# Kernel optimization log

Hardware: AMD Instinct MI355X
Metric: run time of the kernel (lower is better)

## Reference

```python
import jax, jax.numpy as jnp
import numpy as np

B, S, D = 8, 4096, 192
MEM_READ, MEM_WRITE, MEM_READY = 156, 157, 158


def setup_inputs() -> dict:
    key = jax.random.key(0)
    ks = jax.random.split(key, 9)
    inp = {"x": jax.random.normal(ks[0], (B, S, D), dtype=jnp.float32)}
    names = ["Wq_r", "Wk_r", "Wv_r", "Wo_r", "Wq_w", "Wk_w", "Wv_w", "Wo_w"]
    for i, n in enumerate(names):
        inp[n] = jax.random.normal(ks[i + 1], (D, D), dtype=jnp.float32) * 0.02
    return inp


def _attention(x, Wq, Wk, Wv, Wo):
    # single-head, non-causal PureAttention: q/k/v = x @ W.T, softmax(qk^T/sqrt(D)) v, then W_o
    q = jnp.einsum('bsd,ed->bse', x, Wq)
    k = jnp.einsum('bsd,ed->bse', x, Wk)
    v = jnp.einsum('bsd,ed->bse', x, Wv)
    scale = jnp.asarray(1.0 / np.sqrt(D), x.dtype)
    scores = jnp.einsum('bqe,bke->bqk', q, k) * scale  # [B,S,S]
    attn = jax.nn.softmax(scores, axis=-1)
    o = jnp.einsum('bqk,bke->bqe', attn, v)
    return jnp.einsum('bse,oe->bso', o, Wo)


def reference(x, Wq_r, Wk_r, Wv_r, Wo_r, Wq_w, Wk_w, Wv_w, Wo_w):
    read_flag = x[:, 0, MEM_READ]    # [B]
    write_flag = x[:, 0, MEM_WRITE]  # [B]
    read_res = _attention(x, Wq_r, Wk_r, Wv_r, Wo_r)
    write_res = _attention(x, Wq_w, Wk_w, Wv_w, Wo_w)
    rg = read_flag[:, None, None]
    wg = write_flag[:, None, None]
    out = x + rg * (read_res - x) + wg * (write_res - x)
    out = out.at[:, :, MEM_READ].set(0.0)
    out = out.at[:, :, MEM_WRITE].set(0.0)
    ready = (read_flag + write_flag)[:, None]  # broadcast over seq
    out = out.at[:, :, MEM_READY].set(jnp.broadcast_to(ready, out.shape[:2]))
    return out
```

## Files before the change

kernel.cpp:

```cpp
#include <hip/hip_runtime.h>
#include <stdint.h>

#define B_ 8
#define S_ 4096
#define D_ 192
#define M_ (B_*S_)

typedef short v8s __attribute__((ext_vector_type(8)));
typedef float v4f __attribute__((ext_vector_type(4)));
typedef unsigned short v4us __attribute__((ext_vector_type(4)));

static __device__ __forceinline__ unsigned short f2bf(float f){
  union{float f; unsigned u;} v; v.f=f;
  unsigned u = v.u;
  unsigned r = (u + 0x7fffu + ((u>>16)&1u))>>16;
  return (unsigned short)r;
}
static __device__ __forceinline__ float fexp2(float x){
  return __builtin_amdgcn_exp2f(x);
}
static __device__ __forceinline__ unsigned cvtpk(float lo, float hi){
  unsigned r;
  asm("v_cvt_pk_bf16_f32 %0, %1, %2" : "=v"(r) : "v"(lo), "v"(hi));
  return r;
}

typedef const __attribute__((address_space(1))) unsigned int gu32;
typedef __attribute__((address_space(3))) unsigned int lu32;
#define GLL16(gp, lp) __builtin_amdgcn_global_load_lds((gu32*)(gp), (lu32*)(lp), 16, 0, 0)

__global__ void cvt_w_kernel(const float* w0,const float* w1,const float* w2,const float* w3,
                             const float* w4,const float* w5,const float* w6,const float* w7,
                             unsigned short* dst){
  int w = blockIdx.y;
  const float* src;
  switch(w){
    case 0: src=w0; break; case 1: src=w1; break; case 2: src=w2; break; case 3: src=w3; break;
    case 4: src=w4; break; case 5: src=w5; break; case 6: src=w6; break; default: src=w7; break;
  }
  int i = blockIdx.x*256 + threadIdx.x;
  float v = src[i];
  if(w==0 || w==4) v *= 0.10411754211316668f;
  dst[(size_t)w*36864 + i] = f2bf(v);
}

__global__ __launch_bounds__(256) void proj_kernel(
    const float* __restrict__ x, const unsigned short* __restrict__ Wb,
    unsigned short* __restrict__ QKV)
{
  __shared__ __align__(16) unsigned short Vstage[192*72];
  const size_t MD = (size_t)M_*D_;
  int tid = threadIdx.x;
  int wid = tid>>6, lane = tid&63;
  int lr = lane&15, lg = lane>>4, kb = lg*8;
  int m0 = blockIdx.x*64 + wid*16;
  int row = m0 + lr;

  v8s a[6];
  #pragma unroll
  for(int c=0;c<6;c++){
    const float* xp = &x[(size_t)row*D_ + c*32 + kb];
    float4 f0 = *(const float4*)xp;
    float4 f1 = *(const float4*)(xp+4);
    v8s t;
    t[0]=(short)f2bf(f0.x); t[1]=(short)f2bf(f0.y); t[2]=(short)f2bf(f0.z); t[3]=(short)f2bf(f0.w);
    t[4]=(short)f2bf(f1.x); t[5]=(short)f2bf(f1.y); t[6]=(short)f2bf(f1.z); t[7]=(short)f2bf(f1.w);
    a[c]=t;
  }
  int bidx = m0 / S_;
  int sb   = (blockIdx.x*64) % S_;
  int sloc = wid*16 + lg*4;

  for(int path=0; path<2; path++){
    unsigned short* dstQ = QKV + (size_t)path*3*MD;
    for(int which=0; which<2; which++){
      const unsigned short* W = Wb + (size_t)(path*4 + which)*36864;
      unsigned short* dst = which==0 ? dstQ : dstQ + MD;
      #pragma unroll
      for(int nt=0; nt<12; nt++){
        v4f acc = {0.f,0.f,0.f,0.f};
        int n = nt*16 + lr;
        #pragma unroll
        for(int c=0;c<6;c++){
          v8s bfr = *(const v8s*)&W[(size_t)n*D_ + c*32 + kb];
          acc = __builtin_amdgcn_mfma_f32_16x16x32_bf16(a[c], bfr, acc, 0,0,0);
        }
        int col = nt*16 + lr;
        int r0 = m0 + lg*4;
        #pragma unroll
        for(int r=0;r<4;r++) dst[(size_t)(r0+r)*D_ + col] = f2bf(acc[r]);
      }
    }
    {
      const unsigned short* W = Wb + (size_t)(path*4 + 2)*36864;
      #pragma unroll
      for(int nt=0; nt<12; nt++){
        v4f acc = {0.f,0.f,0.f,0.f};
        int n = nt*16 + lr;
        #pragma unroll
        for(int c=0;c<6;c++){
          v8s bfr = *(const v8s*)&W[(size_t)n*D_ + c*32 + kb];
          acc = __builtin_amdgcn_mfma_f32_16x16x32_bf16(a[c], bfr, acc, 0,0,0);
        }
        int col = nt*16 + lr;
        v4us pk;
        pk[0]=f2bf(acc[0]); pk[1]=f2bf(acc[1]); pk[2]=f2bf(acc[2]); pk[3]=f2bf(acc[3]);
        *(v4us*)&Vstage[col*72 + sloc] = pk;
      }
      __syncthreads();
      unsigned short* dstV = dstQ + 2*MD;
      size_t vg = (size_t)bidx*D_*S_ + sb;
      #pragma unroll
      for(int j=0;j<6;j++){
        int i = tid + j*256;
        int d = i>>3, s8 = (i&7)*8;
        *(v8s*)&dstV[vg + (size_t)d*S_ + s8] = *(const v8s*)&Vstage[d*72 + s8];
      }
      __syncthreads();
    }
  }
}

__global__ __launch_bounds__(256,2) void attn_kernel(unsigned short* __restrict__ QKV)
{
  __shared__ __align__(16) unsigned short Kb[2][32*192];
  __shared__ __align__(16) unsigned short Vb[3][192*32];

  int flat = blockIdx.x + 32*blockIdx.y + 256*blockIdx.z;
  int w = (flat&7)*64 + (flat>>3);
  int qi = w & 31;
  int b  = (w>>5) & 7;
  int z  = w>>8;

  const size_t MD = (size_t)M_*D_;
  size_t poff = (size_t)z*3*MD;
  const unsigned short* Q  = QKV + poff;
  const unsigned short* K  = QKV + poff + MD;
  const unsigned short* Vt = QKV + poff + 2*MD;
  unsigned short* O = QKV + poff;

  int q0 = qi*128;
  int tid = threadIdx.x, wid=tid>>6, lane=tid&63;
  int lr = lane&15, lg = lane>>4, kb = lg*8;
  size_t bbase = (size_t)b*S_*D_;
  const size_t vbase = (size_t)b*D_*S_;
  int qrow0 = q0 + wid*32;

  int koff[3], voff[3];
  #pragma unroll
  for(int j=0;j<3;j++){
    int pb = (wid*3+j)*1024 + lane*16;
    int krow = pb/384, kin = pb%384;
    koff[j] = krow*192 + ((kin ^ ((krow&7)<<4))>>1);
    int vrow = pb>>6,  vin = pb&63;
    voff[j] = vrow*4096 + ((vin ^ (((vrow>>1)&3)<<4))>>1);
  }
  int xk = (lr&7)<<4;
  int kco[6];
  #pragma unroll
  for(int c=0;c<6;c++) kco[c] = ((c*64 + lg*16) ^ xk) >> 1;
  int vro = ((lg*16) ^ (((lr>>1)&3)<<4)) >> 1;

  v8s qf[2][6];
  #pragma unroll
  for(int h=0;h<2;h++){
    size_t qrow = bbase + (size_t)(qrow0 + h*16 + lr)*D_;
    #pragma unroll
    for(int c=0;c<6;c++) qf[h][c] = *(const v8s*)&Q[qrow + c*32 + kb];
  }
  float lsum[2] = {0.f, 0.f};
  v4f oacc[2][12];
  #pragma unroll
  for(int h=0;h<2;h++)
    #pragma unroll
    for(int e=0;e<12;e++) oacc[h][e] = (v4f){0.f,0.f,0.f,0.f};

  auto do_qk = [&](int kcur, v4f sacc[2][2]){
    __builtin_amdgcn_s_setprio(1);
    #pragma unroll
    for(int ct=0; ct<2; ct++){
      v4f s0v = {0.f,0.f,0.f,0.f}, s1v = {0.f,0.f,0.f,0.f};
      #pragma unroll
      for(int c=0;c<6;c++){
        v8s kf = *(const v8s*)&Kb[kcur][(ct*16+lr)*192 + kco[c]];
        s0v = __builtin_amdgcn_mfma_f32_16x16x32_bf16(kf, qf[0][c], s0v, 0,0,0);
        s1v = __builtin_amdgcn_mfma_f32_16x16x32_bf16(kf, qf[1][c], s1v, 0,0,0);
      }
      sacc[0][ct]=s0v; sacc[1][ct]=s1v;
    }
    __builtin_amdgcn_s_setprio(0);
  };
  auto do_softmax = [&](v4f sacc[2][2], v8s pa[2]){
    #pragma unroll
    for(int h=0;h<2;h++){
      float p00=fexp2(sacc[h][0][0]), p01=fexp2(sacc[h][0][1]);
      float p02=fexp2(sacc[h][0][2]), p03=fexp2(sacc[h][0][3]);
      float p10=fexp2(sacc[h][1][0]), p11=fexp2(sacc[h][1][1]);
      float p12=fexp2(sacc[h][1][2]), p13=fexp2(sacc[h][1][3]);
      lsum[h] += ((p00+p01)+(p02+p03)) + ((p10+p11)+(p12+p13));
      unsigned X0=cvtpk(p00,p01), X1=cvtpk(p02,p03);
      unsigned Y0=cvtpk(p10,p11), Y1=cvtpk(p12,p13);
      asm("v_permlane32_swap_b32 %0, %1" : "+v"(Y0), "+v"(X0));
      asm("v_permlane32_swap_b32 %0, %1" : "+v"(Y1), "+v"(X1));
      asm("v_permlane16_swap_b32 %0, %1" : "+v"(Y0), "+v"(X0));
      asm("v_permlane16_swap_b32 %0, %1" : "+v"(Y1), "+v"(X1));
      union{ v8s s; unsigned w[4]; } u;
      u.w[0] = X0;  u.w[1] = X1;  u.w[2] = Y0;  u.w[3] = Y1;
      pa[h] = u.s;
    }
  };
  auto do_pv = [&](int vcur, v8s pa[2]){
    __builtin_amdgcn_s_setprio(1);
    #pragma unroll
    for(int e=0;e<12;e++){
      v8s vbf = *(const v8s*)&Vb[vcur][(e*16+lr)*32 + vro];
      oacc[0][e] = __builtin_amdgcn_mfma_f32_16x16x32_bf16(pa[0], vbf, oacc[0][e], 0,0,0);
      oacc[1][e] = __builtin_amdgcn_mfma_f32_16x16x32_bf16(pa[1], vbf, oacc[1][e], 0,0,0);
    }
    __builtin_amdgcn_s_setprio(0);
  };

  #pragma unroll
  for(int j=0;j<3;j++){
    GLL16(K  + bbase + koff[j], &Kb[0][(wid*3+j)*512]);
    GLL16(Vt + vbase + voff[j], &Vb[0][(wid*3+j)*512]);
  }
  asm volatile("s_waitcnt vmcnt(0)" ::: "memory");
  __syncthreads();

  v8s pa_prev[2];
  {
    v4f sacc[2][2];
    do_qk(0, sacc);
    const unsigned short* kg = K  + bbase + (size_t)6144;
    const unsigned short* vg = Vt + vbase + (size_t)32;
    #pragma unroll
    for(int j=0;j<3;j++){
      GLL16(kg + koff[j], &Kb[1][(wid*3+j)*512]);
      GLL16(vg + voff[j], &Vb[1][(wid*3+j)*512]);
    }
    __builtin_amdgcn_sched_barrier(0);
    do_softmax(sacc, pa_prev);
  }

  for(int t=1; t<128; t++){
    asm volatile("s_waitcnt vmcnt(0)" ::: "memory");
    __syncthreads();
    int kcur = t&1;
    int vprev = (t-1)%3, vnext = (t+1)%3;

    v4f sacc[2][2];
    do_qk(kcur, sacc);

    if(t<127){
      const unsigned short* kg = K  + bbase + (size_t)(t+1)*6144;
      const unsigned short* vg = Vt + vbase + (size_t)(t+1)*32;
      #pragma unroll
      for(int j=0;j<3;j++){
        GLL16(kg + koff[j], &Kb[(t+1)&1][(wid*3+j)*512]);
        GLL16(vg + voff[j], &Vb[vnext][(wid*3+j)*512]);
      }
    }
    __builtin_amdgcn_sched_barrier(0);

    do_pv(vprev, pa_prev);
    do_softmax(sacc, pa_prev);
  }
  do_pv(127%3, pa_prev);

  float invr[2][4];
  #pragma unroll
  for(int h=0;h<2;h++){
    float ps = lsum[h];
    ps += __shfl_xor(ps, 16);
    ps += __shfl_xor(ps, 32);
    float iv = 1.0f/ps;
    #pragma unroll
    for(int r=0;r<4;r++) invr[h][r] = __shfl(iv, lg*4+r, 16);
  }
  #pragma unroll
  for(int h=0;h<2;h++){
    size_t orow0 = bbase + (size_t)(qrow0 + h*16 + lg*4)*D_;
    #pragma unroll
    for(int e=0;e<12;e++){
      #pragma unroll
      for(int r=0;r<4;r++){
        O[orow0 + (size_t)r*D_ + e*16 + lr] = f2bf(oacc[h][e][r]*invr[h][r]);
      }
    }
  }
}

__global__ __launch_bounds__(256) void final_kernel(
  const float* __restrict__ x,
  const unsigned short* __restrict__ Or,
  const unsigned short* __restrict__ Ow,
  const unsigned short* __restrict__ WoR,
  const unsigned short* __restrict__ WoW,
  float* __restrict__ out)
{
  int tid=threadIdx.x, wid=tid>>6, lane=tid&63;
  int lr=lane&15, lg=lane>>4, kb=lg*8;
  int m0 = blockIdx.x*64 + wid*16;
  int arow = m0 + lr;
  v8s ar[6], aw[6];
  #pragma unroll
  for(int c=0;c<6;c++){
    ar[c] = *(const v8s*)&Or[(size_t)arow*D_ + c*32 + kb];
    aw[c] = *(const v8s*)&Ow[(size_t)arow*D_ + c*32 + kb];
  }
  int bidx = m0 / S_;
  float rf = x[(size_t)bidx*S_*D_ + 156];
  float wf = x[(size_t)bidx*S_*D_ + 157];
  #pragma unroll
  for(int nt=0; nt<12; nt++){
    v4f accR={0.f,0.f,0.f,0.f}, accW={0.f,0.f,0.f,0.f};
    int n = nt*16 + lr;
    #pragma unroll
    for(int c=0;c<6;c++){
      v8s br = *(const v8s*)&WoR[(size_t)n*D_ + c*32 + kb];
      accR = __builtin_amdgcn_mfma_f32_16x16x32_bf16(ar[c], br, accR,0,0,0);
      v8s bw = *(const v8s*)&WoW[(size_t)n*D_ + c*32 + kb];
      accW = __builtin_amdgcn_mfma_f32_16x16x32_bf16(aw[c], bw, accW,0,0,0);
    }
    #pragma unroll
    for(int r=0;r<4;r++){
      int row = m0 + lg*4 + r;
      int col = nt*16 + lr;
      float xv = x[(size_t)row*D_ + col];
      float val = xv + rf*(accR[r]-xv) + wf*(accW[r]-xv);
      if(col==156||col==157) val = 0.f;
      else if(col==158) val = rf+wf;
      out[(size_t)row*D_ + col] = val;
    }
  }
}

extern "C" void kernel_launch(void* const* d_in, const int* in_sizes, int n_in,
                              void* d_out, int out_size, void* d_ws, size_t ws_size,
                              hipStream_t stream) {
  const float* x = (const float*)d_in[0];
  unsigned short* ws = (unsigned short*)d_ws;
  const size_t WSZ = 36864;
  const size_t MD  = (size_t)M_*D_;
  unsigned short* Wb  = ws;
  unsigned short* QKV = ws + 8*WSZ;

  cvt_w_kernel<<<dim3(144,8),256,0,stream>>>(
      (const float*)d_in[1],(const float*)d_in[2],(const float*)d_in[3],(const float*)d_in[4],
      (const float*)d_in[5],(const float*)d_in[6],(const float*)d_in[7],(const float*)d_in[8], Wb);

  proj_kernel<<<512,256,0,stream>>>(x, Wb, QKV);
  attn_kernel<<<dim3(32,8,2),256,0,stream>>>(QKV);
  final_kernel<<<512,256,0,stream>>>(x, QKV , QKV+3*MD ,
                                     Wb+3*WSZ, Wb+7*WSZ, (float*)d_out);
}
```

Measured before the change: 357.7 us.

## Split attention block into 8 waves of 16 query rows with specialized K/V loaders

The attention kernel moves from 256 threads (4 waves, 32 query rows each) to 512 threads (8 waves, 16 query rows each). Each wave now keeps half the accumulators and Q fragments, which lowers register pressure so the launch bound can ask for more resident blocks. Global-to-LDS staging is split by role: waves 0-3 load K tiles and waves 4-7 load V tiles. The trade-off is that each K/V LDS fragment is reused by fewer MFMAs per wave, so LDS read traffic per FLOP doubles, and the block-wide barrier now spans twice as many waves.

```diff
diff --git a/kernel.cpp b/kernel.cpp
--- a/kernel.cpp
+++ b/kernel.cpp
@@ -121,7 +121,7 @@
   }
 }
 
-__global__ __launch_bounds__(256,2) void attn_kernel(unsigned short* __restrict__ QKV)
+__global__ __launch_bounds__(512,3) void attn_kernel(unsigned short* __restrict__ QKV)
 {
   __shared__ __align__(16) unsigned short Kb[2][32*192];
   __shared__ __align__(16) unsigned short Vb[3][192*32];
@@ -144,16 +144,21 @@
   int lr = lane&15, lg = lane>>4, kb = lg*8;
   size_t bbase = (size_t)b*S_*D_;
   const size_t vbase = (size_t)b*D_*S_;
-  int qrow0 = q0 + wid*32;
-
-  int koff[3], voff[3];
+  int qrow0 = q0 + wid*16;
+
+  bool isK = wid < 4;
+  int cb = (isK ? wid : wid-4)*3;
+  int soff[3];
   #pragma unroll
   for(int j=0;j<3;j++){
-    int pb = (wid*3+j)*1024 + lane*16;
-    int krow = pb/384, kin = pb%384;
-    koff[j] = krow*192 + ((kin ^ ((krow&7)<<4))>>1);
-    int vrow = pb>>6,  vin = pb&63;
-    voff[j] = vrow*4096 + ((vin ^ (((vrow>>1)&3)<<4))>>1);
+    int pb = (cb+j)*1024 + lane*16;
+    if(isK){
+      int krow = pb/384, kin = pb%384;
+      soff[j] = krow*192 + ((kin ^ ((krow&7)<<4))>>1);
+    } else {
+      int vrow = pb>>6,  vin = pb&63;
+      soff[j] = vrow*4096 + ((vin ^ (((vrow>>1)&3)<<4))>>1);
+    }
   }
   int xk = (lr&7)<<4;
   int kco[6];
@@ -161,84 +166,77 @@
   for(int c=0;c<6;c++) kco[c] = ((c*64 + lg*16) ^ xk) >> 1;
   int vro = ((lg*16) ^ (((lr>>1)&3)<<4)) >> 1;
 
-  v8s qf[2][6];
-  #pragma unroll
-  for(int h=0;h<2;h++){
-    size_t qrow = bbase + (size_t)(qrow0 + h*16 + lr)*D_;
-    #pragma unroll
-    for(int c=0;c<6;c++) qf[h][c] = *(const v8s*)&Q[qrow + c*32 + kb];
-  }
-  float lsum[2] = {0.f, 0.f};
-  v4f oacc[2][12];
-  #pragma unroll
-  for(int h=0;h<2;h++)
-    #pragma unroll
-    for(int e=0;e<12;e++) oacc[h][e] = (v4f){0.f,0.f,0.f,0.f};
-
-  auto do_qk = [&](int kcur, v4f sacc[2][2]){
+  v8s qf[6];
+  {
+    size_t qrow = bbase + (size_t)(qrow0 + lr)*D_;
+    #pragma unroll
+    for(int c=0;c<6;c++) qf[c] = *(const v8s*)&Q[qrow + c*32 + kb];
+  }
+  float lsum = 0.f;
+  v4f oacc[12];
+  #pragma unroll
+  for(int e=0;e<12;e++) oacc[e] = (v4f){0.f,0.f,0.f,0.f};
+
+  auto stage = [&](int t, int kbuf, int vbuf){
+    if(isK){
+      const unsigned short* kg = K + bbase + (size_t)t*6144;
+      #pragma unroll
+      for(int j=0;j<3;j++) GLL16(kg + soff[j], &Kb[kbuf][(cb+j)*512]);
+    } else {
+      const unsigned short* vg = Vt + vbase + (size_t)t*32;
+      #pragma unroll
+      for(int j=0;j<3;j++) GLL16(vg + soff[j], &Vb[vbuf][(cb+j)*512]);
+    }
+  };
+  auto do_qk = [&](int kcur, v4f sacc[2]){
     __builtin_amdgcn_s_setprio(1);
     #pragma unroll
     for(int ct=0; ct<2; ct++){
-      v4f s0v = {0.f,0.f,0.f,0.f}, s1v = {0.f,0.f,0.f,0.f};
+      v4f s = {0.f,0.f,0.f,0.f};
       #pragma unroll
       for(int c=0;c<6;c++){
         v8s kf = *(const v8s*)&Kb[kcur][(ct*16+lr)*192 + kco[c]];
-        s0v = __builtin_amdgcn_mfma_f32_16x16x32_bf16(kf, qf[0][c], s0v, 0,0,0);
-        s1v = __builtin_amdgcn_mfma_f32_16x16x32_bf16(kf, qf[1][c], s1v, 0,0,0);
+        s = __builtin_amdgcn_mfma_f32_16x16x32_bf16(kf, qf[c], s, 0,0,0);
       }
-      sacc[0][ct]=s0v; sacc[1][ct]=s1v;
+      sacc[ct]=s;
     }
     __builtin_amdgcn_s_setprio(0);
   };
-  auto do_softmax = [&](v4f sacc[2][2], v8s pa[2]){
-    #pragma unroll
-    for(int h=0;h<2;h++){
-      float p00=fexp2(sacc[h][0][0]), p01=fexp2(sacc[h][0][1]);
-      float p02=fexp2(sacc[h][0][2]), p03=fexp2(sacc[h][0][3]);
-      float p10=fexp2(sacc[h][1][0]), p11=fexp2(sacc[h][1][1]);
-      float p12=fexp2(sacc[h][1][2]), p13=fexp2(sacc[h][1][3]);
-      lsum[h] += ((p00+p01)+(p02+p03)) + ((p10+p11)+(p12+p13));
-      unsigned X0=cvtpk(p00,p01), X1=cvtpk(p02,p03);
-      unsigned Y0=cvtpk(p10,p11), Y1=cvtpk(p12,p13);
-      asm("v_permlane32_swap_b32 %0, %1" : "+v"(Y0), "+v"(X0));
-      asm("v_permlane32_swap_b32 %0, %1" : "+v"(Y1), "+v"(X1));
-      asm("v_permlane16_swap_b32 %0, %1" : "+v"(Y0), "+v"(X0));
-      asm("v_permlane16_swap_b32 %0, %1" : "+v"(Y1), "+v"(X1));
-      union{ v8s s; unsigned w[4]; } u;
-      u.w[0] = X0;  u.w[1] = X1;  u.w[2] = Y0;  u.w[3] = Y1;
-      pa[h] = u.s;
-    }
+  auto do_softmax = [&](v4f sacc[2], v8s& pa){
+    float p00=fexp2(sacc[0][0]), p01=fexp2(sacc[0][1]);
+    float p02=fexp2(sacc[0][2]), p03=fexp2(sacc[0][3]);
+    float p10=fexp2(sacc[1][0]), p11=fexp2(sacc[1][1]);
+    float p12=fexp2(sacc[1][2]), p13=fexp2(sacc[1][3]);
+    lsum += ((p00+p01)+(p02+p03)) + ((p10+p11)+(p12+p13));
+    unsigned X0=cvtpk(p00,p01), X1=cvtpk(p02,p03);
+    unsigned Y0=cvtpk(p10,p11), Y1=cvtpk(p12,p13);
+    asm("v_permlane32_swap_b32 %0, %1" : "+v"(Y0), "+v"(X0));
+    asm("v_permlane32_swap_b32 %0, %1" : "+v"(Y1), "+v"(X1));
+    asm("v_permlane16_swap_b32 %0, %1" : "+v"(Y0), "+v"(X0));
+    asm("v_permlane16_swap_b32 %0, %1" : "+v"(Y1), "+v"(X1));
+    union{ v8s s; unsigned w[4]; } u;
+    u.w[0] = X0;  u.w[1] = X1;  u.w[2] = Y0;  u.w[3] = Y1;
+    pa = u.s;
   };
-  auto do_pv = [&](int vcur, v8s pa[2]){
+  auto do_pv = [&](int vcur, v8s pa){
     __builtin_amdgcn_s_setprio(1);
     #pragma unroll
     for(int e=0;e<12;e++){
       v8s vbf = *(const v8s*)&Vb[vcur][(e*16+lr)*32 + vro];
-      oacc[0][e] = __builtin_amdgcn_mfma_f32_16x16x32_bf16(pa[0], vbf, oacc[0][e], 0,0,0);
-      oacc[1][e] = __builtin_amdgcn_mfma_f32_16x16x32_bf16(pa[1], vbf, oacc[1][e], 0,0,0);
+      oacc[e] = __builtin_amdgcn_mfma_f32_16x16x32_bf16(pa, vbf, oacc[e], 0,0,0);
     }
     __builtin_amdgcn_s_setprio(0);
   };
 
-  #pragma unroll
-  for(int j=0;j<3;j++){
-    GLL16(K  + bbase + koff[j], &Kb[0][(wid*3+j)*512]);
-    GLL16(Vt + vbase + voff[j], &Vb[0][(wid*3+j)*512]);
-  }
+  stage(0, 0, 0);
   asm volatile("s_waitcnt vmcnt(0)" ::: "memory");
   __syncthreads();
 
-  v8s pa_prev[2];
+  v8s pa_prev;
   {
-    v4f sacc[2][2];
+    v4f sacc[2];
     do_qk(0, sacc);
-    const unsigned short* kg = K  + bbase + (size_t)6144;
-    const unsigned short* vg = Vt + vbase + (size_t)32;
-    #pragma unroll
-    for(int j=0;j<3;j++){
-      GLL16(kg + koff[j], &Kb[1][(wid*3+j)*512]);
-      GLL16(vg + voff[j], &Vb[1][(wid*3+j)*512]);
-    }
+    stage(1, 1, 1);
     __builtin_amdgcn_sched_barrier(0);
     do_softmax(sacc, pa_prev);
   }
@@ -246,47 +244,28 @@
   for(int t=1; t<128; t++){
     asm volatile("s_waitcnt vmcnt(0)" ::: "memory");
     __syncthreads();
-    int kcur = t&1;
-    int vprev = (t-1)%3, vnext = (t+1)%3;
-
-    v4f sacc[2][2];
-    do_qk(kcur, sacc);
-
-    if(t<127){
-      const unsigned short* kg = K  + bbase + (size_t)(t+1)*6144;
-      const unsigned short* vg = Vt + vbase + (size_t)(t+1)*32;
-      #pragma unroll
-      for(int j=0;j<3;j++){
-        GLL16(kg + koff[j], &Kb[(t+1)&1][(wid*3+j)*512]);
-        GLL16(vg + voff[j], &Vb[vnext][(wid*3+j)*512]);
-      }
-    }
+    v4f sacc[2];
+    do_qk(t&1, sacc);
+    if(t<127) stage(t+1, (t+1)&1, (t+1)%3);
     __builtin_amdgcn_sched_barrier(0);
-
-    do_pv(vprev, pa_prev);
+    do_pv((t-1)%3, pa_prev);
     do_softmax(sacc, pa_prev);
   }
   do_pv(127%3, pa_prev);
 
-  float invr[2][4];
-  #pragma unroll
-  for(int h=0;h<2;h++){
-    float ps = lsum[h];
-    ps += __shfl_xor(ps, 16);
-    ps += __shfl_xor(ps, 32);
-    float iv = 1.0f/ps;
-    #pragma unroll
-    for(int r=0;r<4;r++) invr[h][r] = __shfl(iv, lg*4+r, 16);
-  }
-  #pragma unroll
-  for(int h=0;h<2;h++){
-    size_t orow0 = bbase + (size_t)(qrow0 + h*16 + lg*4)*D_;
-    #pragma unroll
-    for(int e=0;e<12;e++){
-      #pragma unroll
-      for(int r=0;r<4;r++){
-        O[orow0 + (size_t)r*D_ + e*16 + lr] = f2bf(oacc[h][e][r]*invr[h][r]);
-      }
+  float ps = lsum;
+  ps += __shfl_xor(ps, 16);
+  ps += __shfl_xor(ps, 32);
+  float iv = 1.0f/ps;
+  float invr[4];
+  #pragma unroll
+  for(int r=0;r<4;r++) invr[r] = __shfl(iv, lg*4+r, 16);
+  size_t orow0 = bbase + (size_t)(qrow0 + lg*4)*D_;
+  #pragma unroll
+  for(int e=0;e<12;e++){
+    #pragma unroll
+    for(int r=0;r<4;r++){
+      O[orow0 + (size_t)r*D_ + e*16 + lr] = f2bf(oacc[e][r]*invr[r]);
     }
   }
 }
@@ -351,7 +330,7 @@
       (const float*)d_in[5],(const float*)d_in[6],(const float*)d_in[7],(const float*)d_in[8], Wb);
 
   proj_kernel<<<512,256,0,stream>>>(x, Wb, QKV);
-  attn_kernel<<<dim3(32,8,2),256,0,stream>>>(QKV);
+  attn_kernel<<<dim3(32,8,2),512,0,stream>>>(QKV);
   final_kernel<<<512,256,0,stream>>>(x, QKV , QKV+3*MD ,
                                      Wb+3*WSZ, Wb+7*WSZ, (float*)d_out);
 }
```

New measurement: 356.8 us. No clear change (-0.2%).

## Quantize Q and K to FP8 and use FP8 MFMA for attention scores

Applied to the files above, without the earlier changes.

Q and K projections are now stored as FP8 (with the softmax scale split evenly across Wq and Wk) and QK^T uses the fp8 MFMA, halving K/Q bytes moved and LDS footprint. K is staged through registers into padded LDS, V uses a double buffer instead of a triple buffer, and the pipeline is simplified to compute QK, softmax and PV for the same tile each iteration, with occupancy raised to three blocks per SM. The goal is to cut memory traffic and MFMA cost in the score computation, at the price of lower score precision and less overlap between softmax and PV.

```diff
diff --git a/kernel.cpp b/kernel.cpp
--- a/kernel.cpp
+++ b/kernel.cpp
@@ -9,6 +9,7 @@
 typedef short v8s __attribute__((ext_vector_type(8)));
 typedef float v4f __attribute__((ext_vector_type(4)));
 typedef unsigned short v4us __attribute__((ext_vector_type(4)));
+typedef unsigned long long ull;
 
 static __device__ __forceinline__ unsigned short f2bf(float f){
   union{float f; unsigned u;} v; v.f=f;
@@ -23,6 +24,34 @@
   unsigned r;
   asm("v_cvt_pk_bf16_f32 %0, %1, %2" : "=v"(r) : "v"(lo), "v"(hi));
   return r;
+}
+
+static __device__ __forceinline__ unsigned sw_fp8(float x){
+  union{float f; unsigned u;} v; v.f = x;
+  unsigned s = (v.u >> 24) & 0x80u;
+  float a = fabsf(x);
+  if (a < 0.001953125f) return s;
+  if (a >= 240.f) return s | 0x7Eu;
+  if (a < 0.015625f) {
+    int m = (int)(a*512.f + 0.5f); if(m>7) m=7;
+    return s | (unsigned)m;
+  }
+  int e = (int)((v.u >> 23) & 0xff) - 127;
+  unsigned mant = (v.u >> 20) & 0x7u;
+  unsigned rest = v.u & 0xFFFFFu;
+  if (rest > 0x80000u || (rest == 0x80000u && (mant&1u))) mant++;
+  unsigned ee = (unsigned)(e + 7);
+  if (mant == 8u){ mant = 0u; ee++; }
+  return s | (ee<<3) | mant;
+}
+template<bool HI>
+static __device__ __forceinline__ unsigned pk8(float a, float b, unsigned old){
+#if __has_builtin(__builtin_amdgcn_cvt_pk_fp8_f32)
+  return __builtin_amdgcn_cvt_pk_fp8_f32(a, b, old, HI);
+#else
+  unsigned p = sw_fp8(a) | (sw_fp8(b)<<8);
+  return HI ? ((old & 0x0000FFFFu) | (p<<16)) : ((old & 0xFFFF0000u) | p);
+#endif
 }
 
 typedef const __attribute__((address_space(1))) unsigned int gu32;
@@ -40,16 +69,17 @@
   }
   int i = blockIdx.x*256 + threadIdx.x;
   float v = src[i];
-  if(w==0 || w==4) v *= 0.10411754211316668f;
+  if(w==0 || w==4 || w==1 || w==5) v *= 0.32267249f;
   dst[(size_t)w*36864 + i] = f2bf(v);
 }
 
 __global__ __launch_bounds__(256) void proj_kernel(
     const float* __restrict__ x, const unsigned short* __restrict__ Wb,
-    unsigned short* __restrict__ QKV)
+    unsigned char* __restrict__ QK8, unsigned short* __restrict__ V16)
 {
   __shared__ __align__(16) unsigned short Vstage[192*72];
-  const size_t MD = (size_t)M_*D_;
+  const size_t MDB = (size_t)M_*D_;
+  const size_t MD  = (size_t)M_*D_;
   int tid = threadIdx.x;
   int wid = tid>>6, lane = tid&63;
   int lr = lane&15, lg = lane>>4, kb = lg*8;
@@ -72,10 +102,10 @@
   int sloc = wid*16 + lg*4;
 
   for(int path=0; path<2; path++){
-    unsigned short* dstQ = QKV + (size_t)path*3*MD;
+    unsigned char* dstQ8 = QK8 + (size_t)path*2*MDB;
     for(int which=0; which<2; which++){
       const unsigned short* W = Wb + (size_t)(path*4 + which)*36864;
-      unsigned short* dst = which==0 ? dstQ : dstQ + MD;
+      unsigned char* dst = which==0 ? dstQ8 : dstQ8 + MDB;
       #pragma unroll
       for(int nt=0; nt<12; nt++){
         v4f acc = {0.f,0.f,0.f,0.f};
@@ -88,7 +118,10 @@
         int col = nt*16 + lr;
         int r0 = m0 + lg*4;
         #pragma unroll
-        for(int r=0;r<4;r++) dst[(size_t)(r0+r)*D_ + col] = f2bf(acc[r]);
+        for(int r=0;r<4;r++){
+          unsigned p = pk8<false>(acc[r], 0.f, 0u);
+          dst[(size_t)(r0+r)*D_ + col] = (unsigned char)(p & 0xFF);
+        }
       }
     }
     {
@@ -108,7 +141,7 @@
         *(v4us*)&Vstage[col*72 + sloc] = pk;
       }
       __syncthreads();
-      unsigned short* dstV = dstQ + 2*MD;
+      unsigned short* dstV = V16 + (size_t)path*MD;
       size_t vg = (size_t)bidx*D_*S_ + sb;
       #pragma unroll
       for(int j=0;j<6;j++){
@@ -121,10 +154,15 @@
   }
 }
 
-__global__ __launch_bounds__(256,2) void attn_kernel(unsigned short* __restrict__ QKV)
+#define KSTR8 200
+
+__global__ __launch_bounds__(256,3) void attn_kernel(
+    const unsigned char* __restrict__ QK8,
+    const unsigned short* __restrict__ V16,
+    unsigned short* __restrict__ Ob)
 {
-  __shared__ __align__(16) unsigned short Kb[2][32*192];
-  __shared__ __align__(16) unsigned short Vb[3][192*32];
+  __shared__ __align__(16) unsigned char  KL[2][32*KSTR8];
+  __shared__ __align__(16) unsigned short VL[2][192*32];
 
   int flat = blockIdx.x + 32*blockIdx.y + 256*blockIdx.z;
   int w = (flat&7)*64 + (flat>>3);
@@ -132,41 +170,37 @@
   int b  = (w>>5) & 7;
   int z  = w>>8;
 
-  const size_t MD = (size_t)M_*D_;
-  size_t poff = (size_t)z*3*MD;
-  const unsigned short* Q  = QKV + poff;
-  const unsigned short* K  = QKV + poff + MD;
-  const unsigned short* Vt = QKV + poff + 2*MD;
-  unsigned short* O = QKV + poff;
+  const size_t MDB = (size_t)M_*D_;
+  const unsigned char* Q8 = QK8 + (size_t)z*2*MDB;
+  const unsigned char* K8 = Q8 + MDB;
+  const unsigned short* Vt = V16 + (size_t)z*M_*D_;
+  unsigned short* O = Ob + (size_t)z*M_*D_;
 
   int q0 = qi*128;
   int tid = threadIdx.x, wid=tid>>6, lane=tid&63;
-  int lr = lane&15, lg = lane>>4, kb = lg*8;
-  size_t bbase = (size_t)b*S_*D_;
-  const size_t vbase = (size_t)b*D_*S_;
+  int lr = lane&15, lg = lane>>4;
+  size_t bK = (size_t)b*S_*D_;
+  size_t bV = (size_t)b*D_*S_;
   int qrow0 = q0 + wid*32;
 
-  int koff[3], voff[3];
+  int ksR = tid>>3, ksC = (tid&7)*24;
+  int kLds = ksR*KSTR8 + ksC;
+  int voff[3], vLds[3];
   #pragma unroll
   for(int j=0;j<3;j++){
-    int pb = (wid*3+j)*1024 + lane*16;
-    int krow = pb/384, kin = pb%384;
-    koff[j] = krow*192 + ((kin ^ ((krow&7)<<4))>>1);
-    int vrow = pb>>6,  vin = pb&63;
+    int i = tid + j*256;
+    int vrow = i>>2, vin = (i&3)*16;
     voff[j] = vrow*4096 + ((vin ^ (((vrow>>1)&3)<<4))>>1);
-  }
-  int xk = (lr&7)<<4;
-  int kco[6];
-  #pragma unroll
-  for(int c=0;c<6;c++) kco[c] = ((c*64 + lg*16) ^ xk) >> 1;
+    vLds[j] = i*16;
+  }
   int vro = ((lg*16) ^ (((lr>>1)&3)<<4)) >> 1;
 
-  v8s qf[2][6];
+  long qf8[2][6];
   #pragma unroll
   for(int h=0;h<2;h++){
-    size_t qrow = bbase + (size_t)(qrow0 + h*16 + lr)*D_;
-    #pragma unroll
-    for(int c=0;c<6;c++) qf[h][c] = *(const v8s*)&Q[qrow + c*32 + kb];
+    const unsigned char* qp = Q8 + bK + (size_t)(qrow0 + h*16 + lr)*D_;
+    #pragma unroll
+    for(int c=0;c<6;c++) qf8[h][c] = *(const long*)(qp + c*32 + lg*8);
   }
   float lsum[2] = {0.f, 0.f};
   v4f oacc[2][12];
@@ -175,18 +209,37 @@
     #pragma unroll
     for(int e=0;e<12;e++) oacc[h][e] = (v4f){0.f,0.f,0.f,0.f};
 
+  ull kreg0, kreg1, kreg2;
+  auto kissue = [&](int t){
+    const unsigned char* kg = K8 + bK + (size_t)t*6144 + ksR*192 + ksC;
+    kreg0 = *(const ull*)(kg);
+    kreg1 = *(const ull*)(kg+8);
+    kreg2 = *(const ull*)(kg+16);
+  };
+  auto kwrite = [&](int buf){
+    unsigned char* d = &KL[buf][kLds];
+    *(ull*)(d)    = kreg0;
+    *(ull*)(d+8)  = kreg1;
+    *(ull*)(d+16) = kreg2;
+  };
+  auto vissue = [&](int t, int buf){
+    const unsigned short* vg = Vt + bV + (size_t)t*32;
+    #pragma unroll
+    for(int j=0;j<3;j++) GLL16(vg + voff[j], ((unsigned char*)&VL[buf][0]) + vLds[j]);
+  };
   auto do_qk = [&](int kcur, v4f sacc[2][2]){
     __builtin_amdgcn_s_setprio(1);
     #pragma unroll
     for(int ct=0; ct<2; ct++){
-      v4f s0v = {0.f,0.f,0.f,0.f}, s1v = {0.f,0.f,0.f,0.f};
+      v4f s0 = {0.f,0.f,0.f,0.f}, s1 = {0.f,0.f,0.f,0.f};
+      const unsigned char* rb = &KL[kcur][(ct*16+lr)*KSTR8];
       #pragma unroll
       for(int c=0;c<6;c++){
-        v8s kf = *(const v8s*)&Kb[kcur][(ct*16+lr)*192 + kco[c]];
-        s0v = __builtin_amdgcn_mfma_f32_16x16x32_bf16(kf, qf[0][c], s0v, 0,0,0);
-        s1v = __builtin_amdgcn_mfma_f32_16x16x32_bf16(kf, qf[1][c], s1v, 0,0,0);
-      }
-      sacc[0][ct]=s0v; sacc[1][ct]=s1v;
+        long kf8 = *(const long*)(rb + c*32 + lg*8);
+        s0 = __builtin_amdgcn_mfma_f32_16x16x32_fp8_fp8(kf8, qf8[0][c], s0, 0,0,0);
+        s1 = __builtin_amdgcn_mfma_f32_16x16x32_fp8_fp8(kf8, qf8[1][c], s1, 0,0,0);
+      }
+      sacc[0][ct]=s0; sacc[1][ct]=s1;
     }
     __builtin_amdgcn_s_setprio(0);
   };
@@ -213,60 +266,34 @@
     __builtin_amdgcn_s_setprio(1);
     #pragma unroll
     for(int e=0;e<12;e++){
-      v8s vbf = *(const v8s*)&Vb[vcur][(e*16+lr)*32 + vro];
+      v8s vbf = *(const v8s*)&VL[vcur][(e*16+lr)*32 + vro];
       oacc[0][e] = __builtin_amdgcn_mfma_f32_16x16x32_bf16(pa[0], vbf, oacc[0][e], 0,0,0);
       oacc[1][e] = __builtin_amdgcn_mfma_f32_16x16x32_bf16(pa[1], vbf, oacc[1][e], 0,0,0);
     }
     __builtin_amdgcn_s_setprio(0);
   };
 
-  #pragma unroll
-  for(int j=0;j<3;j++){
-    GLL16(K  + bbase + koff[j], &Kb[0][(wid*3+j)*512]);
-    GLL16(Vt + vbase + voff[j], &Vb[0][(wid*3+j)*512]);
-  }
+  kissue(0);
+  vissue(0, 0);
+  kwrite(0);
   asm volatile("s_waitcnt vmcnt(0)" ::: "memory");
   __syncthreads();
 
-  v8s pa_prev[2];
-  {
+  for(int t=0; t<128; t++){
+    int cur = t&1;
+    if(t<127){ kissue(t+1); vissue(t+1, cur^1); }
+    __builtin_amdgcn_sched_barrier(0);
+
     v4f sacc[2][2];
-    do_qk(0, sacc);
-    const unsigned short* kg = K  + bbase + (size_t)6144;
-    const unsigned short* vg = Vt + vbase + (size_t)32;
-    #pragma unroll
-    for(int j=0;j<3;j++){
-      GLL16(kg + koff[j], &Kb[1][(wid*3+j)*512]);
-      GLL16(vg + voff[j], &Vb[1][(wid*3+j)*512]);
-    }
-    __builtin_amdgcn_sched_barrier(0);
-    do_softmax(sacc, pa_prev);
-  }
-
-  for(int t=1; t<128; t++){
+    do_qk(cur, sacc);
+    v8s pa[2];
+    do_softmax(sacc, pa);
+    do_pv(cur, pa);
+
+    if(t<127) kwrite(cur^1);
     asm volatile("s_waitcnt vmcnt(0)" ::: "memory");
     __syncthreads();
-    int kcur = t&1;
-    int vprev = (t-1)%3, vnext = (t+1)%3;
-
-    v4f sacc[2][2];
-    do_qk(kcur, sacc);
-
-    if(t<127){
-      const unsigned short* kg = K  + bbase + (size_t)(t+1)*6144;
-      const unsigned short* vg = Vt + vbase + (size_t)(t+1)*32;
-      #pragma unroll
-      for(int j=0;j<3;j++){
-        GLL16(kg + koff[j], &Kb[(t+1)&1][(wid*3+j)*512]);
-        GLL16(vg + voff[j], &Vb[vnext][(wid*3+j)*512]);
-      }
-    }
-    __builtin_amdgcn_sched_barrier(0);
-
-    do_pv(vprev, pa_prev);
-    do_softmax(sacc, pa_prev);
-  }
-  do_pv(127%3, pa_prev);
+  }
 
   float invr[2][4];
   #pragma unroll
@@ -280,7 +307,7 @@
   }
   #pragma unroll
   for(int h=0;h<2;h++){
-    size_t orow0 = bbase + (size_t)(qrow0 + h*16 + lg*4)*D_;
+    size_t orow0 = ((size_t)b*S_ + qrow0 + h*16 + lg*4)*D_;
     #pragma unroll
     for(int e=0;e<12;e++){
       #pragma unroll
@@ -340,18 +367,20 @@
                               void* d_out, int out_size, void* d_ws, size_t ws_size,
                               hipStream_t stream) {
   const float* x = (const float*)d_in[0];
-  unsigned short* ws = (unsigned short*)d_ws;
+  char* wsb = (char*)d_ws;
   const size_t WSZ = 36864;
-  const size_t MD  = (size_t)M_*D_;
-  unsigned short* Wb  = ws;
-  unsigned short* QKV = ws + 8*WSZ;
+  const size_t MDB = (size_t)M_*D_;
+  unsigned short* Wb  = (unsigned short*)wsb;
+  unsigned char*  QK8 = (unsigned char*)(wsb + 8*WSZ*2);
+  unsigned short* V16 = (unsigned short*)(wsb + 8*WSZ*2 + 4*MDB);
+  unsigned short* Ob  = V16 + 2*MDB;
 
   cvt_w_kernel<<<dim3(144,8),256,0,stream>>>(
       (const float*)d_in[1],(const float*)d_in[2],(const float*)d_in[3],(const float*)d_in[4],
       (const float*)d_in[5],(const float*)d_in[6],(const float*)d_in[7],(const float*)d_in[8], Wb);
 
-  proj_kernel<<<512,256,0,stream>>>(x, Wb, QKV);
-  attn_kernel<<<dim3(32,8,2),256,0,stream>>>(QKV);
-  final_kernel<<<512,256,0,stream>>>(x, QKV , QKV+3*MD ,
+  proj_kernel<<<512,256,0,stream>>>(x, Wb, QK8, V16);
+  attn_kernel<<<dim3(32,8,2),256,0,stream>>>(QK8, V16, Ob);
+  final_kernel<<<512,256,0,stream>>>(x, Ob, Ob + MDB,
                                      Wb+3*WSZ, Wb+7*WSZ, (float*)d_out);
 }
```

After: 354.4 us. Within noise of the previous version (-0.9%).
